# Kernel optimization log

Measured on AMD Instinct MI355X. Metric: run time of the kernel, lower is better.

The kernel has to match this reference:

```python
import jax, jax.numpy as jnp
import numpy as np

N_NODES = 50000
N_EDGES = 800000
IN_FEATS, N_HIDDEN, OUT_FEATS = 512, 512, 256


def setup_inputs() -> dict:
    key = jax.random.key(0)
    ks = jax.random.split(key, 10)
    features = jax.random.normal(ks[0], (N_NODES, IN_FEATS), dtype=jnp.float32)
    src = jax.random.randint(ks[1], (N_EDGES,), 0, N_NODES, dtype=jnp.int64)
    dst = jax.random.randint(ks[2], (N_EDGES,), 0, N_NODES, dtype=jnp.int64)
    def glorot(k, fan_in, fan_out):
        s = jnp.sqrt(6.0 / (fan_in + fan_out)).astype(jnp.float32)
        return jax.random.uniform(k, (fan_in, fan_out), jnp.float32, -s, s)
    W0 = glorot(ks[3], IN_FEATS, N_HIDDEN)
    b0 = jnp.zeros((N_HIDDEN,), jnp.float32)
    W1 = glorot(ks[4], N_HIDDEN, N_HIDDEN)
    b1 = jnp.zeros((N_HIDDEN,), jnp.float32)
    W2 = glorot(ks[5], N_HIDDEN, OUT_FEATS)
    b2 = jnp.zeros((OUT_FEATS,), jnp.float32)
    return {"features": features, "src": src, "dst": dst,
            "W0": W0, "b0": b0, "W1": W1, "b1": b1, "W2": W2, "b2": b2}


def _graph_conv(x, W, b, src, dst, out_norm, in_norm, activation):
    # DGL GraphConv, norm='both': D_out^{-1/2} A^T D_in^{-1/2}? -> per-node scale,
    # gather on src, segment-sum on dst, scale, linear, bias, activation.
    h = x @ W                               # [N, out] dense GEMM (weight applied first)
    h = h * out_norm[:, None]               # src-side degree norm
    msgs = h[src]                           # [E, out] gather
    agg = jax.ops.segment_sum(msgs, dst, num_segments=x.shape[0])  # [N, out]
    agg = agg * in_norm[:, None] + b
    return activation(agg) if activation is not None else agg


def reference(features, src, dst, W0, b0, W1, b1, W2, b2):
    n = features.shape[0]
    ones = jnp.ones((src.shape[0],), jnp.float32)
    out_deg = jnp.clip(jax.ops.segment_sum(ones, src, num_segments=n), 1.0)
    in_deg = jnp.clip(jax.ops.segment_sum(ones, dst, num_segments=n), 1.0)
    out_norm = jax.lax.rsqrt(out_deg)
    in_norm = jax.lax.rsqrt(in_deg)
    # eval mode: dropout between layers is identity
    h = _graph_conv(features, W0, b0, src, dst, out_norm, in_norm, jax.nn.relu)
    h = _graph_conv(h, W1, b1, src, dst, out_norm, in_norm, jax.nn.relu)
    h = _graph_conv(h, W2, b2, src, dst, out_norm, in_norm, None)
    return h
```

## Files before the change

kernel.cpp:

```cpp
#include <hip/hip_runtime.h>

#define N_NODES 50000
#define N_EDGES 800000

typedef __attribute__((ext_vector_type(8))) _Float16 half8;
typedef __attribute__((ext_vector_type(4))) float f32x4;
typedef __attribute__((ext_vector_type(8))) unsigned short ushort8;

static __device__ __forceinline__ unsigned short f2h(float f) {
    _Float16 h = (_Float16)f;
    return __builtin_bit_cast(unsigned short, h);
}
static __device__ __forceinline__ float h2f(unsigned short u) {
    return (float)__builtin_bit_cast(_Float16, u);
}

static __device__ __forceinline__ void async16(unsigned short* lds, const unsigned short* g) {
    __builtin_amdgcn_global_load_lds(
        (const __attribute__((address_space(1))) void*)g,
        (__attribute__((address_space(3))) void*)lds, 16, 0, 0);
}

__global__ void hist_kernel(const int* __restrict__ src, const int* __restrict__ dst,
                            int* __restrict__ outc, int* __restrict__ inc) {
    int i = blockIdx.x * blockDim.x + threadIdx.x;
    if (i < N_EDGES) {
        atomicAdd(&outc[src[i]], 1);
        atomicAdd(&inc[dst[i]], 1);
    }
}

__global__ void norm_kernel(const int* __restrict__ outc, const int* __restrict__ inc,
                            float* __restrict__ outn, float* __restrict__ inn) {
    int i = blockIdx.x * blockDim.x + threadIdx.x;
    if (i < N_NODES) {
        outn[i] = rsqrtf(fmaxf((float)outc[i], 1.0f));
        inn[i]  = rsqrtf(fmaxf((float)inc[i], 1.0f));
    }
}

__global__ __launch_bounds__(256) void scan1(const int* __restrict__ cnt,
                                             int* __restrict__ row_start,
                                             int* __restrict__ bsum, int n) {
    __shared__ int t[256];
    int tid = threadIdx.x;
    int i = blockIdx.x * 256 + tid;
    int v = (i < n) ? cnt[i] : 0;
    t[tid] = v;
    __syncthreads();
#pragma unroll
    for (int off = 1; off < 256; off <<= 1) {
        int x = (tid >= off) ? t[tid - off] : 0;
        __syncthreads();
        t[tid] += x;
        __syncthreads();
    }
    if (i < n) row_start[i] = t[tid] - v;
    if (tid == 255) bsum[blockIdx.x] = t[255];
}

__global__ __launch_bounds__(256) void scan2(int* __restrict__ bsum,
                                             int* __restrict__ boff,
                                             int* __restrict__ row_start, int nb) {
    __shared__ int t[256];
    int tid = threadIdx.x;
    int v = (tid < nb) ? bsum[tid] : 0;
    t[tid] = v;
    __syncthreads();
#pragma unroll
    for (int off = 1; off < 256; off <<= 1) {
        int x = (tid >= off) ? t[tid - off] : 0;
        __syncthreads();
        t[tid] += x;
        __syncthreads();
    }
    if (tid < nb) boff[tid] = t[tid] - v;
    if (tid == 0) row_start[N_NODES] = N_EDGES;
}

__global__ __launch_bounds__(256) void scan3(int* __restrict__ row_start,
                                             const int* __restrict__ boff, int n) {
    int i = blockIdx.x * 256 + threadIdx.x;
    if (i < n) row_start[i] += boff[blockIdx.x];
}

__global__ __launch_bounds__(256) void bucket_hist(const int* __restrict__ inc,
                                                   int* __restrict__ bcnt) {
    __shared__ int lh[1024];
    int tid = threadIdx.x;
    for (int b = tid; b < 1024; b += 256) lh[b] = 0;
    __syncthreads();
    int i = blockIdx.x * 256 + tid;
    if (i < N_NODES) atomicAdd(&lh[min(inc[i], 1023)], 1);
    __syncthreads();
    for (int b = tid; b < 1024; b += 256) {
        int v = lh[b];
        if (v) atomicAdd(&bcnt[b], v);
    }
}

__global__ __launch_bounds__(1024) void bucket_scan(const int* __restrict__ bcnt,
                                                    int* __restrict__ boff2) {
    __shared__ int t[1024];
    int tid = threadIdx.x;
    int v = bcnt[tid];
    t[tid] = v;
    __syncthreads();
#pragma unroll
    for (int off = 1; off < 1024; off <<= 1) {
        int x = (tid >= off) ? t[tid - off] : 0;
        __syncthreads();
        t[tid] += x;
        __syncthreads();
    }
    boff2[tid] = t[tid] - v;
}

__global__ __launch_bounds__(256) void bucket_scatter(const int* __restrict__ inc,
                               int* __restrict__ bcur,
                               int* __restrict__ porder, int* __restrict__ rank,
                               int* __restrict__ pdeg) {
    __shared__ int lcnt[1024];
    __shared__ int gbase[1024];
    int tid = threadIdx.x;
    for (int b = tid; b < 1024; b += 256) lcnt[b] = 0;
    __syncthreads();
    int i = blockIdx.x * 256 + tid;
    int deg = 0, bkt = 0, lpos = 0;
    if (i < N_NODES) {
        deg = inc[i];
        bkt = min(deg, 1023);
        lpos = atomicAdd(&lcnt[bkt], 1);
    }
    __syncthreads();
    for (int b = tid; b < 1024; b += 256) {
        int v = lcnt[b];
        if (v) gbase[b] = atomicAdd(&bcur[b], v);
    }
    __syncthreads();
    if (i < N_NODES) {
        int p = gbase[bkt] + lpos;
        porder[p] = i;
        rank[i] = p;
        pdeg[p] = deg;
    }
}

__global__ void fill_kernel(const int* __restrict__ src, const int* __restrict__ dst,
                            const int* __restrict__ rank, const int* __restrict__ prow,
                            int* __restrict__ cursor, int* __restrict__ csr2) {
    int e = blockIdx.x * blockDim.x + threadIdx.x;
    if (e < N_EDGES) {
        int d = dst[e];
        int pos = atomicAdd(&cursor[d], 1);
        csr2[prow[rank[d]] + pos] = src[e];
    }
}

__global__ __launch_bounds__(256) void conv_W(const float* __restrict__ W,
                                              unsigned short* __restrict__ Wt,
                                              int K, int N) {
    __shared__ float t[32][33];
    int tx = threadIdx.x & 31, ty = threadIdx.x >> 5;
    int kb = blockIdx.x * 32, nb = blockIdx.y * 32;
#pragma unroll
    for (int i = 0; i < 4; ++i)
        t[ty + 8 * i][tx] = W[(size_t)(kb + ty + 8 * i) * N + nb + tx];
    __syncthreads();
#pragma unroll
    for (int i = 0; i < 4; ++i) {
        float v = t[tx][ty + 8 * i];
        int n = nb + ty + 8 * i, k = kb + tx;
        Wt[(size_t)n * K + k] = f2h(v);
    }
}

__global__ void conv_A(const float4* __restrict__ feat4, const float* __restrict__ outn,
                       ushort4* __restrict__ Af, long total4) {
    long i = (long)blockIdx.x * blockDim.x + threadIdx.x;
    if (i >= total4) return;
    int row = (int)(i >> 7);
    float s = outn[row];
    float4 v = feat4[i];
    ushort4 h;
    h.x = f2h(v.x * s);
    h.y = f2h(v.y * s);
    h.z = f2h(v.z * s);
    h.w = f2h(v.w * s);
    Af[i] = h;
}

__global__ __launch_bounds__(256) void gemm_mfma(
    const unsigned short* __restrict__ A, const unsigned short* __restrict__ B,
    unsigned short* __restrict__ C, int M, int N)
{
    const int K = 512;
    __shared__ unsigned short sA[128 * 32];
    __shared__ unsigned short sB[128 * 32];

    const int tid = threadIdx.x;
    const int rowBase = blockIdx.x * 128;
    const int colBase = blockIdx.y * 128;
    const int wave = tid >> 6;
    const int lane = tid & 63;
    const int wr = (wave >> 1) * 64;
    const int wc = (wave & 1) * 64;
    const int lrow = lane & 15;
    const int quad = lane >> 4;

    f32x4 acc[4][4] = {};

    const int crow = tid >> 2;
    const int ck   = (tid & 3) * 8;
    const int ar0 = min(rowBase + crow, M - 1);
    const int ar1 = min(rowBase + 64 + crow, M - 1);
    const int bn0 = colBase + crow;
    const int bn1 = colBase + 64 + crow;
    const int ldsOf0 = tid * 8;
    const int ldsOf1 = 64 * 32 + tid * 8;

    for (int k0 = 0; k0 < K; k0 += 32) {
        __syncthreads();
        async16(sA + ldsOf0, A + (size_t)ar0 * K + k0 + ck);
        async16(sA + ldsOf1, A + (size_t)ar1 * K + k0 + ck);
        async16(sB + ldsOf0, B + (size_t)bn0 * K + k0 + ck);
        async16(sB + ldsOf1, B + (size_t)bn1 * K + k0 + ck);
        __syncthreads();

        half8 av[4], bv[4];
#pragma unroll
        for (int mt = 0; mt < 4; ++mt)
            av[mt] = *(const half8*)&sA[(wr + mt * 16 + lrow) * 32 + quad * 8];
#pragma unroll
        for (int nt = 0; nt < 4; ++nt)
            bv[nt] = *(const half8*)&sB[(wc + nt * 16 + lrow) * 32 + quad * 8];
#pragma unroll
        for (int mt = 0; mt < 4; ++mt)
#pragma unroll
            for (int nt = 0; nt < 4; ++nt)
                acc[mt][nt] = __builtin_amdgcn_mfma_f32_16x16x32_f16(av[mt], bv[nt], acc[mt][nt], 0, 0, 0);
    }

#pragma unroll
    for (int mt = 0; mt < 4; ++mt) {
        int grow0 = rowBase + wr + mt * 16 + quad * 4;
#pragma unroll
        for (int nt = 0; nt < 4; ++nt) {
            int gcol = colBase + wc + nt * 16 + lrow;
            size_t chunkBase = (size_t)(gcol >> 5) * M * 32 + (gcol & 31);
#pragma unroll
            for (int r = 0; r < 4; ++r) {
                int grow = grow0 + r;
                if (grow < M) C[chunkBase + (size_t)grow * 32] = f2h(acc[mt][nt][r]);
            }
        }
    }
}

#define SLAB 1024

__global__ __launch_bounds__(256) void agg_f16_v4(
    const unsigned short* __restrict__ H, const int* __restrict__ csr2,
    const int* __restrict__ porder, const int* __restrict__ prow,
    const float* __restrict__ inn, const float* __restrict__ outn,
    const float* __restrict__ bias, unsigned short* __restrict__ Af)
{
    __shared__ int sIdx[4][SLAB];
    const int tid = threadIdx.x, lane = tid & 63, w = tid >> 6;
    const int s = lane >> 2, f = lane & 3;
    const int c = blockIdx.z * 8 + blockIdx.x;
    const int t = blockIdx.y * 64 + w * 16 + s;

    int d = 0, st = N_EDGES, en = N_EDGES;
    if (t < N_NODES) {
        d  = porder[t];
        st = prow[t];
        en = prow[t + 1];
    }
    const int eStart = __shfl(st, 0);
    const int eEnd   = __shfl(en, 63);

    const unsigned short* Hc = H + (size_t)c * (N_NODES * 32);
    int* slab = sIdx[w];
    float a[8] = {};

    for (int b = eStart; b < eEnd; b += SLAB) {
        const int nstage = min(eEnd - b, SLAB);
        for (int i = lane; i < nstage; i += 64)
            slab[i] = __builtin_nontemporal_load(csr2 + b + i);
        asm volatile("s_waitcnt lgkmcnt(0)" ::: "memory");

        const int js = max(st, b);
        const int je = min(en, b + nstage);
#pragma unroll 4
        for (int k = js; k < je; ++k) {
            int idx = slab[k - b];
            const ushort8 u = *(const ushort8*)(Hc + (unsigned)idx * 32u + (unsigned)f * 8u);
#pragma unroll
            for (int q = 0; q < 8; ++q) a[q] += h2f(u[q]);
        }
        asm volatile("" ::: "memory");
    }

    if (t < N_NODES) {
        float si = inn[d], so = outn[d];
        float b8[8];
        *(float4*)&b8[0] = *(const float4*)(bias + c * 32 + f * 8);
        *(float4*)&b8[4] = *(const float4*)(bias + c * 32 + f * 8 + 4);
        ushort8 h;
#pragma unroll
        for (int q = 0; q < 8; ++q)
            h[q] = f2h(fmaxf(a[q] * si + b8[q], 0.f) * so);
        __builtin_nontemporal_store(h,
            (ushort8*)(Af + (size_t)d * 512 + c * 32 + f * 8));
    }
}

__global__ __launch_bounds__(256) void agg_f32_v4(
    const unsigned short* __restrict__ H, const int* __restrict__ csr2,
    const int* __restrict__ porder, const int* __restrict__ prow,
    const float* __restrict__ inn, const float* __restrict__ bias,
    float* __restrict__ out)
{
    __shared__ int sIdx[4][SLAB];
    const int tid = threadIdx.x, lane = tid & 63, w = tid >> 6;
    const int s = lane >> 2, f = lane & 3;
    const int c = blockIdx.x;
    const int t = blockIdx.y * 64 + w * 16 + s;

    int d = 0, st = N_EDGES, en = N_EDGES;
    if (t < N_NODES) {
        d  = porder[t];
        st = prow[t];
        en = prow[t + 1];
    }
    const int eStart = __shfl(st, 0);
    const int eEnd   = __shfl(en, 63);

    const unsigned short* Hc = H + (size_t)c * (N_NODES * 32);
    int* slab = sIdx[w];
    float a[8] = {};

    for (int b = eStart; b < eEnd; b += SLAB) {
        const int nstage = min(eEnd - b, SLAB);
        for (int i = lane; i < nstage; i += 64)
            slab[i] = __builtin_nontemporal_load(csr2 + b + i);
        asm volatile("s_waitcnt lgkmcnt(0)" ::: "memory");

        const int js = max(st, b);
        const int je = min(en, b + nstage);
#pragma unroll 4
        for (int k = js; k < je; ++k) {
            int idx = slab[k - b];
            const ushort8 u = *(const ushort8*)(Hc + (unsigned)idx * 32u + (unsigned)f * 8u);
#pragma unroll
            for (int q = 0; q < 8; ++q) a[q] += h2f(u[q]);
        }
        asm volatile("" ::: "memory");
    }

    if (t < N_NODES) {
        float si = inn[d];
        float b8[8];
        *(float4*)&b8[0] = *(const float4*)(bias + c * 32 + f * 8);
        *(float4*)&b8[4] = *(const float4*)(bias + c * 32 + f * 8 + 4);
        f32x4 r0, r1;
        r0.x = a[0] * si + b8[0]; r0.y = a[1] * si + b8[1];
        r0.z = a[2] * si + b8[2]; r0.w = a[3] * si + b8[3];
        r1.x = a[4] * si + b8[4]; r1.y = a[5] * si + b8[5];
        r1.z = a[6] * si + b8[6]; r1.w = a[7] * si + b8[7];
        float* op = out + (size_t)d * 256 + c * 32 + f * 8;
        __builtin_nontemporal_store(r0, (f32x4*)op);
        __builtin_nontemporal_store(r1, (f32x4*)(op + 4));
    }
}

extern "C" void kernel_launch(void* const* d_in, const int* in_sizes, int n_in,
                              void* d_out, int out_size, void* d_ws, size_t ws_size,
                              hipStream_t stream) {
    const float* feat = (const float*)d_in[0];
    const int*   src  = (const int*)d_in[1];
    const int*   dst  = (const int*)d_in[2];
    const float* W0   = (const float*)d_in[3];
    const float* b0   = (const float*)d_in[4];
    const float* W1   = (const float*)d_in[5];
    const float* b1   = (const float*)d_in[6];
    const float* W2   = (const float*)d_in[7];
    const float* b2   = (const float*)d_in[8];
    float* out = (float*)d_out;

    char* p = (char*)d_ws;
    auto alloc = [&](size_t bytes) {
        char* r = p;
        p += (bytes + 63) & ~(size_t)63;
        return r;
    };
    float* outn = (float*)alloc(N_NODES * 4);
    float* inn  = (float*)alloc(N_NODES * 4);
    int* outc      = (int*)alloc(N_NODES * 4);
    int* inc       = (int*)alloc(N_NODES * 4);
    int* cursor    = (int*)alloc(N_NODES * 4);
    int* bcnt      = (int*)alloc(1024 * 4);
    int* porder    = (int*)alloc(N_NODES * 4);
    int* rank      = (int*)alloc(N_NODES * 4);
    int* pdeg      = (int*)alloc(N_NODES * 4);
    int* prow      = (int*)alloc((N_NODES + 1) * 4);
    int* bsum      = (int*)alloc(256 * 4);
    int* boff      = (int*)alloc(256 * 4);
    int* boff2     = (int*)alloc(1024 * 4);
    int* csr2      = (int*)alloc(N_EDGES * 4);
    unsigned short* W0t = (unsigned short*)alloc(512 * 512 * 2);
    unsigned short* W1t = (unsigned short*)alloc(512 * 512 * 2);
    unsigned short* W2t = (unsigned short*)alloc(256 * 512 * 2);
    unsigned short* Af  = (unsigned short*)alloc((size_t)N_NODES * 512 * 2);
    unsigned short* H   = (unsigned short*)alloc((size_t)N_NODES * 512 * 2);

    const int NB = (N_NODES + 255) / 256;

    hipMemsetAsync(outc, 0, (size_t)3 * N_NODES * 4 + 1024 * 4, stream);
    hist_kernel<<<(N_EDGES + 255) / 256, 256, 0, stream>>>(src, dst, outc, inc);
    norm_kernel<<<(N_NODES + 255) / 256, 256, 0, stream>>>(outc, inc, outn, inn);
    bucket_hist<<<NB, 256, 0, stream>>>(inc, bcnt);
    bucket_scan<<<1, 1024, 0, stream>>>(bcnt, boff2);
    bucket_scatter<<<NB, 256, 0, stream>>>(inc, boff2, porder, rank, pdeg);
    scan1<<<NB, 256, 0, stream>>>(pdeg, prow, bsum, N_NODES);
    scan2<<<1, 256, 0, stream>>>(bsum, boff, prow, NB);
    scan3<<<NB, 256, 0, stream>>>(prow, boff, N_NODES);
    fill_kernel<<<(N_EDGES + 255) / 256, 256, 0, stream>>>(src, dst, rank, prow, cursor, csr2);

    conv_W<<<dim3(16, 16), 256, 0, stream>>>(W0, W0t, 512, 512);
    conv_W<<<dim3(16, 16), 256, 0, stream>>>(W1, W1t, 512, 512);
    conv_W<<<dim3(16, 8),  256, 0, stream>>>(W2, W2t, 512, 256);

    long total4 = (long)N_NODES * 128;
    conv_A<<<(int)((total4 + 255) / 256), 256, 0, stream>>>(
        (const float4*)feat, outn, (ushort4*)Af, total4);

    dim3 g512((N_NODES + 127) / 128, 4);
    dim3 g256((N_NODES + 127) / 128, 2);
    const int NTB = (N_NODES + 63) / 64;
    dim3 gAgg512(8, NTB, 2);
    dim3 gAgg256(8, NTB, 1);

    gemm_mfma<<<g512, 256, 0, stream>>>(Af, W0t, H, N_NODES, 512);
    agg_f16_v4<<<gAgg512, 256, 0, stream>>>(
        H, csr2, porder, prow, inn, outn, b0, Af);

    gemm_mfma<<<g512, 256, 0, stream>>>(Af, W1t, H, N_NODES, 512);
    agg_f16_v4<<<gAgg512, 256, 0, stream>>>(
        H, csr2, porder, prow, inn, outn, b1, Af);

    gemm_mfma<<<g256, 256, 0, stream>>>(Af, W2t, H, N_NODES, 256);
    agg_f32_v4<<<gAgg256, 256, 0, stream>>>(
        H, csr2, porder, prow, inn, b2, out);
}
```

Measured before the change: 725.2 us.

## Process two feature chunks per block and unroll gathers by eight

The 512-wide aggregation kernel now handles two 32-column chunks per block (c0 and c0+8), so each staged slab of CSR indices in LDS serves twice as many gathers and the grid's z dimension goes away. Both aggregation kernels replace the unroll-4 inner loop with an explicit 8-way batch that issues eight independent 16-byte loads before accumulating, to raise memory-level parallelism. Blocks are also walked in reverse node order, presumably so the heavy-degree buckets start first for better tail balance. The cost is fewer blocks in the grid and higher register pressure from two accumulators and eight in-flight vectors.

Measured after the change: 729.1 us. Within noise of the previous version (+0.5%).

```diff
diff --git a/kernel.cpp b/kernel.cpp
--- a/kernel.cpp
+++ b/kernel.cpp
@@ -259,7 +259,38 @@
 
 #define SLAB 1024
 
-__global__ __launch_bounds__(256) void agg_f16_v4(
+#define GATHER8(ACC, HSRC, K0)                                                  \
+    {                                                                           \
+        int i0 = slab[(K0) + 0], i1 = slab[(K0) + 1];                           \
+        int i2 = slab[(K0) + 2], i3 = slab[(K0) + 3];                           \
+        int i4 = slab[(K0) + 4], i5 = slab[(K0) + 5];                           \
+        int i6 = slab[(K0) + 6], i7 = slab[(K0) + 7];                           \
+        const ushort8 u0 = *(const ushort8*)(HSRC + (unsigned)i0 * 32u + fo);   \
+        const ushort8 u1 = *(const ushort8*)(HSRC + (unsigned)i1 * 32u + fo);   \
+        const ushort8 u2 = *(const ushort8*)(HSRC + (unsigned)i2 * 32u + fo);   \
+        const ushort8 u3 = *(const ushort8*)(HSRC + (unsigned)i3 * 32u + fo);   \
+        const ushort8 u4 = *(const ushort8*)(HSRC + (unsigned)i4 * 32u + fo);   \
+        const ushort8 u5 = *(const ushort8*)(HSRC + (unsigned)i5 * 32u + fo);   \
+        const ushort8 u6 = *(const ushort8*)(HSRC + (unsigned)i6 * 32u + fo);   \
+        const ushort8 u7 = *(const ushort8*)(HSRC + (unsigned)i7 * 32u + fo);   \
+        _Pragma("unroll")                                                       \
+        for (int q = 0; q < 8; ++q) {                                           \
+            ACC[q] += h2f(u0[q]); ACC[q] += h2f(u1[q]);                         \
+            ACC[q] += h2f(u2[q]); ACC[q] += h2f(u3[q]);                         \
+            ACC[q] += h2f(u4[q]); ACC[q] += h2f(u5[q]);                         \
+            ACC[q] += h2f(u6[q]); ACC[q] += h2f(u7[q]);                         \
+        }                                                                       \
+    }
+
+#define GATHER1(ACC, HSRC, K0)                                                  \
+    {                                                                           \
+        int idx = slab[(K0)];                                                   \
+        const ushort8 u = *(const ushort8*)(HSRC + (unsigned)idx * 32u + fo);   \
+        _Pragma("unroll")                                                       \
+        for (int q = 0; q < 8; ++q) ACC[q] += h2f(u[q]);                        \
+    }
+
+__global__ __launch_bounds__(256) void agg_f16_v7(
     const unsigned short* __restrict__ H, const int* __restrict__ csr2,
     const int* __restrict__ porder, const int* __restrict__ prow,
     const float* __restrict__ inn, const float* __restrict__ outn,
@@ -268,8 +299,10 @@
     __shared__ int sIdx[4][SLAB];
     const int tid = threadIdx.x, lane = tid & 63, w = tid >> 6;
     const int s = lane >> 2, f = lane & 3;
-    const int c = blockIdx.z * 8 + blockIdx.x;
-    const int t = blockIdx.y * 64 + w * 16 + s;
+    const unsigned fo = (unsigned)f * 8u;
+    const int c0 = blockIdx.x;
+    const int ty = (int)gridDim.y - 1 - (int)blockIdx.y;
+    const int t = ty * 64 + w * 16 + s;
 
     int d = 0, st = N_EDGES, en = N_EDGES;
     if (t < N_NODES) {
@@ -280,9 +313,10 @@
     const int eStart = __shfl(st, 0);
     const int eEnd   = __shfl(en, 63);
 
-    const unsigned short* Hc = H + (size_t)c * (N_NODES * 32);
+    const unsigned short* Hc0 = H + (size_t)c0 * (N_NODES * 32);
+    const unsigned short* Hc1 = H + (size_t)(c0 + 8) * (N_NODES * 32);
     int* slab = sIdx[w];
-    float a[8] = {};
+    float a0[8] = {}, a1[8] = {};
 
     for (int b = eStart; b < eEnd; b += SLAB) {
         const int nstage = min(eEnd - b, SLAB);
@@ -292,31 +326,37 @@
 
         const int js = max(st, b);
         const int je = min(en, b + nstage);
-#pragma unroll 4
-        for (int k = js; k < je; ++k) {
-            int idx = slab[k - b];
-            const ushort8 u = *(const ushort8*)(Hc + (unsigned)idx * 32u + (unsigned)f * 8u);
-#pragma unroll
-            for (int q = 0; q < 8; ++q) a[q] += h2f(u[q]);
-        }
+        int k = js;
+        for (; k + 8 <= je; k += 8) GATHER8(a0, Hc0, k - b);
+        for (; k < je; ++k) GATHER1(a0, Hc0, k - b);
+        k = js;
+        for (; k + 8 <= je; k += 8) GATHER8(a1, Hc1, k - b);
+        for (; k < je; ++k) GATHER1(a1, Hc1, k - b);
         asm volatile("" ::: "memory");
     }
 
     if (t < N_NODES) {
         float si = inn[d], so = outn[d];
         float b8[8];
-        *(float4*)&b8[0] = *(const float4*)(bias + c * 32 + f * 8);
-        *(float4*)&b8[4] = *(const float4*)(bias + c * 32 + f * 8 + 4);
         ushort8 h;
+        *(float4*)&b8[0] = *(const float4*)(bias + c0 * 32 + f * 8);
+        *(float4*)&b8[4] = *(const float4*)(bias + c0 * 32 + f * 8 + 4);
 #pragma unroll
         for (int q = 0; q < 8; ++q)
-            h[q] = f2h(fmaxf(a[q] * si + b8[q], 0.f) * so);
+            h[q] = f2h(fmaxf(a0[q] * si + b8[q], 0.f) * so);
         __builtin_nontemporal_store(h,
-            (ushort8*)(Af + (size_t)d * 512 + c * 32 + f * 8));
-    }
-}
-
-__global__ __launch_bounds__(256) void agg_f32_v4(
+            (ushort8*)(Af + (size_t)d * 512 + c0 * 32 + f * 8));
+        *(float4*)&b8[0] = *(const float4*)(bias + (c0 + 8) * 32 + f * 8);
+        *(float4*)&b8[4] = *(const float4*)(bias + (c0 + 8) * 32 + f * 8 + 4);
+#pragma unroll
+        for (int q = 0; q < 8; ++q)
+            h[q] = f2h(fmaxf(a1[q] * si + b8[q], 0.f) * so);
+        __builtin_nontemporal_store(h,
+            (ushort8*)(Af + (size_t)d * 512 + (c0 + 8) * 32 + f * 8));
+    }
+}
+
+__global__ __launch_bounds__(256) void agg_f32_v7(
     const unsigned short* __restrict__ H, const int* __restrict__ csr2,
     const int* __restrict__ porder, const int* __restrict__ prow,
     const float* __restrict__ inn, const float* __restrict__ bias,
@@ -325,8 +365,10 @@
     __shared__ int sIdx[4][SLAB];
     const int tid = threadIdx.x, lane = tid & 63, w = tid >> 6;
     const int s = lane >> 2, f = lane & 3;
+    const unsigned fo = (unsigned)f * 8u;
     const int c = blockIdx.x;
-    const int t = blockIdx.y * 64 + w * 16 + s;
+    const int ty = (int)gridDim.y - 1 - (int)blockIdx.y;
+    const int t = ty * 64 + w * 16 + s;
 
     int d = 0, st = N_EDGES, en = N_EDGES;
     if (t < N_NODES) {
@@ -349,13 +391,9 @@
 
         const int js = max(st, b);
         const int je = min(en, b + nstage);
-#pragma unroll 4
-        for (int k = js; k < je; ++k) {
-            int idx = slab[k - b];
-            const ushort8 u = *(const ushort8*)(Hc + (unsigned)idx * 32u + (unsigned)f * 8u);
-#pragma unroll
-            for (int q = 0; q < 8; ++q) a[q] += h2f(u[q]);
-        }
+        int k = js;
+        for (; k + 8 <= je; k += 8) GATHER8(a, Hc, k - b);
+        for (; k < je; ++k) GATHER1(a, Hc, k - b);
         asm volatile("" ::: "memory");
     }
 
@@ -439,18 +477,18 @@
     dim3 g512((N_NODES + 127) / 128, 4);
     dim3 g256((N_NODES + 127) / 128, 2);
     const int NTB = (N_NODES + 63) / 64;
-    dim3 gAgg512(8, NTB, 2);
-    dim3 gAgg256(8, NTB, 1);
+    dim3 gAgg512(8, NTB);
+    dim3 gAgg256(8, NTB);
 
     gemm_mfma<<<g512, 256, 0, stream>>>(Af, W0t, H, N_NODES, 512);
-    agg_f16_v4<<<gAgg512, 256, 0, stream>>>(
+    agg_f16_v7<<<gAgg512, 256, 0, stream>>>(
         H, csr2, porder, prow, inn, outn, b0, Af);
 
     gemm_mfma<<<g512, 256, 0, stream>>>(Af, W1t, H, N_NODES, 512);
-    agg_f16_v4<<<gAgg512, 256, 0, stream>>>(
+    agg_f16_v7<<<gAgg512, 256, 0, stream>>>(
         H, csr2, porder, prow, inn, outn, b1, Af);
 
     gemm_mfma<<<g256, 256, 0, stream>>>(Af, W2t, H, N_NODES, 256);
-    agg_f32_v4<<<gAgg256, 256, 0, stream>>>(
+    agg_f32_v7<<<gAgg256, 256, 0, stream>>>(
         H, csr2, porder, prow, inn, b2, out);
 }
```
